# Kernel optimization log

Hardware: AMD Instinct MI355X
Metric: run time of the kernel (lower is better)

## Reference

```python
import jax, jax.numpy as jnp
import numpy as np

V, D, T_CTX, NB, H = 32000, 1024, 2048, 4, 16
HD = D // H  # head_dim (attn_dim // num_heads with attn_dim = model_dim)
B, T = 1, 2048
EPS = 1e-5


def layernorm(x, g, b):
    m = jnp.mean(x, axis=-1, keepdims=True)
    v = jnp.mean((x - m) ** 2, axis=-1, keepdims=True)
    return (x - m) * jax.lax.rsqrt(v + EPS) * g + b


def setup_inputs() -> dict:
    key = jax.random.key(0)
    ks = iter(jax.random.split(key, 64))
    s = 0.02
    inp = {
        "x": jax.random.randint(next(ks), (B, T), 0, V, dtype=jnp.int64 if jax.config.read('jax_enable_x64') else jnp.int32),
        "tok_emb": jax.random.normal(next(ks), (V, D), jnp.float32) * s,
        "pos_emb": jax.random.normal(next(ks), (T_CTX, D), jnp.float32) * s,
        # per-block stacked params, leading dim = num_blocks
        "wq": jax.random.normal(next(ks), (NB, H, D, HD), jnp.float32) * s,
        "bq": jnp.zeros((NB, H, HD), jnp.float32),
        "wk": jax.random.normal(next(ks), (NB, H, D, HD), jnp.float32) * s,
        "bk": jnp.zeros((NB, H, HD), jnp.float32),
        "wv": jax.random.normal(next(ks), (NB, H, D, HD), jnp.float32) * s,
        "bv": jnp.zeros((NB, H, HD), jnp.float32),
        "ln1_g": jnp.ones((NB, D), jnp.float32),
        "ln1_b": jnp.zeros((NB, D), jnp.float32),
        "ln2_g": jnp.ones((NB, D), jnp.float32),
        "ln2_b": jnp.zeros((NB, D), jnp.float32),
        "w1": jax.random.normal(next(ks), (NB, D, 4 * D), jnp.float32) * s,
        "b1": jnp.zeros((NB, 4 * D), jnp.float32),
        "w2": jax.random.normal(next(ks), (NB, 4 * D, D), jnp.float32) * s,
        "b2": jnp.zeros((NB, D), jnp.float32),
        "lnf_g": jnp.ones((D,), jnp.float32),
        "lnf_b": jnp.zeros((D,), jnp.float32),
        "w_vocab": jax.random.normal(next(ks), (D, V), jnp.float32) * s,
        "b_vocab": jnp.zeros((V,), jnp.float32),
    }
    return inp


def reference(x, tok_emb, pos_emb, wq, bq, wk, bk, wv, bv,
              ln1_g, ln1_b, ln2_g, ln2_b, w1, b1, w2, b2,
              lnf_g, lnf_b, w_vocab, b_vocab):
    Bb, Tt = x.shape
    h = tok_emb[x] + pos_emb[:Tt][None, :, :]  # [B,T,D]
    scale = 1.0 / jnp.sqrt(jnp.float32(D))      # NOTE: scaled by embed_dim, as in source
    causal = jnp.tril(jnp.ones((Tt, Tt), bool))
    for l in range(NB):
        xn = layernorm(h, ln1_g[l], ln1_b[l])
        q = jnp.einsum('btd,hdk->bhtk', xn, wq[l]) + bq[l][None, :, None, :]
        k = jnp.einsum('btd,hdk->bhtk', xn, wk[l]) + bk[l][None, :, None, :]
        v = jnp.einsum('btd,hdk->bhtk', xn, wv[l]) + bv[l][None, :, None, :]
        scores = jnp.einsum('bhtk,bhsk->bhts', q, k) * scale
        scores = jnp.where(causal[None, None], scores, -jnp.inf)
        probs = jax.nn.softmax(scores, axis=-1)
        attn = jnp.einsum('bhts,bhsk->bhtk', probs, v)  # [B,H,T,HD]
        attn = attn.transpose(0, 2, 1, 3).reshape(Bb, Tt, H * HD)  # head concat
        h = h + attn
        xn2 = layernorm(h, ln2_g[l], ln2_b[l])
        ff = jax.nn.relu(xn2 @ w1[l] + b1[l]) @ w2[l] + b2[l]
        h = h + ff
    h = layernorm(h, lnf_g, lnf_b)
    logits = h @ w_vocab + b_vocab  # [B,T,V]
    return logits
```

## Files before the change

### kernel.cpp

```cpp
#include <hip/hip_runtime.h>

#define TSEQ 2048
#define DM   1024
#define NBLK 4
#define NHEAD 16
#define HDIM 64
#define DFF  4096
#define NVOC 32000

typedef unsigned short u16;
typedef __attribute__((ext_vector_type(8))) short short8;
typedef __attribute__((ext_vector_type(4))) float f32x4;

__device__ float g_h[TSEQ * DM];
__device__ u16 g_xnh[TSEQ * DM];
__device__ u16 g_xnl[TSEQ * DM];
__device__ u16 g_ffh[TSEQ * DFF];
__device__ u16 g_ffl[TSEQ * DFF];
__device__ u16 g_qh[TSEQ * DM], g_ql[TSEQ * DM];
__device__ u16 g_kh[TSEQ * DM], g_kl[TSEQ * DM];
__device__ u16 g_vth[DM * TSEQ], g_vtl[DM * TSEQ];
__device__ u16 g_wqkvh[NBLK * 3 * DM * DM];
__device__ u16 g_wqkvl[NBLK * 3 * DM * DM];
__device__ u16 g_w1h[NBLK * DM * DFF];
__device__ u16 g_w1l[NBLK * DM * DFF];
__device__ u16 g_w2h[NBLK * DFF * DM];
__device__ u16 g_w2l[NBLK * DFF * DM];
__device__ u16 g_wvh[NVOC * DM];
__device__ u16 g_wvl[NVOC * DM];
__device__ float g_bqkv[NBLK * 3 * DM];

__device__ __forceinline__ u16 f2bf(float x) {
  union { float f; unsigned u; } v; v.f = x;
  unsigned r = (v.u >> 16) & 1u;
  return (u16)((v.u + 0x7fffu + r) >> 16);
}
__device__ __forceinline__ float b2f(u16 h) {
  union { float f; unsigned u; } v; v.u = ((unsigned)h) << 16; return v.f;
}
__device__ __forceinline__ void load16(const u16* g, u16* l) {
  __builtin_amdgcn_global_load_lds(
      (const __attribute__((address_space(1))) unsigned int*)(const void*)g,
      (__attribute__((address_space(3))) unsigned int*)(void*)l, 16, 0, 0);
}

__device__ __forceinline__ const u16* wsel_h(int s) {
  switch (s) { case 0: return g_wqkvh; case 1: return g_w1h;
               case 2: return g_w2h;   default: return g_wvh; }
}
__device__ __forceinline__ const u16* wsel_l(int s) {
  switch (s) { case 0: return g_wqkvl; case 1: return g_w1l;
               case 2: return g_w2l;   default: return g_wvl; }
}

__global__ __launch_bounds__(256) void embed_kernel(const int* __restrict__ x,
                                                    const float* __restrict__ tok,
                                                    const float* __restrict__ pos) {
  int t = blockIdx.x;
  const float* trow = tok + (long)x[t] * DM;
  const float* prow = pos + (long)t * DM;
  float* hrow = g_h + (long)t * DM;
  for (int i = threadIdx.x; i < DM; i += 256)
    hrow[i] = trow[i] + prow[i];
}

__global__ __launch_bounds__(256) void ln_kernel(const float* __restrict__ gamma,
                                                 const float* __restrict__ beta) {
  int t = blockIdx.x;
  const float* xr = g_h + (long)t * DM;
  float s = 0.f, ss = 0.f;
  for (int i = threadIdx.x; i < DM; i += 256) {
    float v = xr[i];
    s += v; ss += v * v;
  }
#pragma unroll
  for (int off = 32; off; off >>= 1) {
    s  += __shfl_down(s, off);
    ss += __shfl_down(ss, off);
  }
  __shared__ float red[2][4];
  int w = threadIdx.x >> 6;
  if ((threadIdx.x & 63) == 0) { red[0][w] = s; red[1][w] = ss; }
  __syncthreads();
  s  = red[0][0] + red[0][1] + red[0][2] + red[0][3];
  ss = red[1][0] + red[1][1] + red[1][2] + red[1][3];
  float mean = s * (1.f / DM);
  float var  = ss * (1.f / DM) - mean * mean;
  float rstd = rsqrtf(var + 1e-5f);
  for (int i = threadIdx.x; i < DM; i += 256) {
    float xv = (xr[i] - mean) * rstd * gamma[i] + beta[i];
    long o = (long)t * DM + i;
    u16 h = f2bf(xv);
    g_xnh[o] = h;
    g_xnl[o] = f2bf(xv - b2f(h));
  }
}

__global__ __launch_bounds__(256) void wsplit_t(const float* __restrict__ src,
                                                int dsel, long doff,
                                                int K, long sD, long sH) {
  __shared__ float tile[64][65];
  u16* dh = const_cast<u16*>(wsel_h(dsel)) + doff;
  u16* dl = const_cast<u16*>(wsel_l(dsel)) + doff;
  int n0 = blockIdx.x * 64, k0 = blockIdx.y * 64;
  int tid = threadIdx.x, ln = tid & 63, sub = tid >> 6;
  const float* sbase = src + (long)(n0 >> 6) * sH + ln;
#pragma unroll
  for (int r = 0; r < 16; ++r) {
    int kk = sub * 16 + r;
    tile[kk][ln] = sbase[(long)(k0 + kk) * sD];
  }
  __syncthreads();
#pragma unroll
  for (int r = 0; r < 16; ++r) {
    int nn = sub * 16 + r;
    float v = tile[ln][nn];
    long o = (long)(n0 + nn) * K + k0 + ln;
    u16 h = f2bf(v);
    dh[o] = h;
    dl[o] = f2bf(v - b2f(h));
  }
}

__global__ __launch_bounds__(256) void bias_qkv(const float* __restrict__ bq,
                                                const float* __restrict__ bk,
                                                const float* __restrict__ bv) {
  int i = blockIdx.x * 256 + threadIdx.x;
  int l = i / (3 * DM);
  int j = i % (3 * DM);
  const float* s = (j < DM) ? bq : (j < 2 * DM) ? bk : bv;
  g_bqkv[i] = s[(long)l * DM + (j & (DM - 1))];
}

template <int BM>
__global__ __launch_bounds__(256) void gemm_mfma(
    int aSel, int wSel, long woff,
    const float* __restrict__ biasPtr, long boff, float* __restrict__ Cout,
    int N, int K, int relu, int outmode) {
  constexpr int WR = BM / 64;
  constexpr int WC = 4 / WR;
  constexpr int NR = 128 / (16 * WC);
  __shared__ __align__(16) u16 lA[2][2][BM * 32];
  __shared__ __align__(16) u16 lB[2][2][128 * 32];

  const u16* Ah = aSel ? g_ffh : g_xnh;
  const u16* Al = aSel ? g_ffl : g_xnl;
  const u16* Bh = wsel_h(wSel) + woff;
  const u16* Bl = wsel_l(wSel) + woff;
  const float* bias = biasPtr ? biasPtr : (g_bqkv + boff);

  const int tid = threadIdx.x;
  const int w = tid >> 6, lane = tid & 63;
  const int wr = w / WC, wc = w % WC;
  const int m0 = blockIdx.x * BM;
  const int n0 = blockIdx.y * 128;
  const int klane = (lane >> 4) * 8;

  long aoff[WR], boffv[2];
#pragma unroll
  for (int i = 0; i < WR; ++i)
    aoff[i] = (long)(m0 + (i * 4 + w) * 16 + (lane & 15)) * K + klane;
#pragma unroll
  for (int i = 0; i < 2; ++i)
    boffv[i] = (long)(n0 + (i * 4 + w) * 16 + (lane & 15)) * K + klane;

  f32x4 acc[4][NR] = {};

  auto STAGE = [&](int k0, int d) {
#pragma unroll
    for (int i = 0; i < WR; ++i) {
      load16(Ah + aoff[i] + k0, &lA[d][0][(i * 4 + w) * 512]);
      load16(Al + aoff[i] + k0, &lA[d][1][(i * 4 + w) * 512]);
    }
#pragma unroll
    for (int i = 0; i < 2; ++i) {
      load16(Bh + boffv[i] + k0, &lB[d][0][(i * 4 + w) * 512]);
      load16(Bl + boffv[i] + k0, &lB[d][1][(i * 4 + w) * 512]);
    }
  };

  STAGE(0, 0);
  __syncthreads();
  int cur = 0;

  for (int k0 = 0; k0 < K; k0 += 32) {
    if (k0 + 32 < K) STAGE(k0 + 32, cur ^ 1);

    const u16* pa0 = &lA[cur][0][(wr * 4) * 512 + lane * 8];
    const u16* pa1 = &lA[cur][1][(wr * 4) * 512 + lane * 8];
    const u16* pb0 = &lB[cur][0][(wc * NR) * 512 + lane * 8];
    const u16* pb1 = &lB[cur][1][(wc * NR) * 512 + lane * 8];

    short8 a[4][2], b[NR][2];
#pragma unroll
    for (int mi = 0; mi < 4; ++mi) {
      a[mi][0] = *(const short8*)(const void*)(pa0 + mi * 512);
      a[mi][1] = *(const short8*)(const void*)(pa1 + mi * 512);
    }
#pragma unroll
    for (int ni = 0; ni < NR; ++ni) {
      b[ni][0] = *(const short8*)(const void*)(pb0 + ni * 512);
      b[ni][1] = *(const short8*)(const void*)(pb1 + ni * 512);
    }
#pragma unroll
    for (int mi = 0; mi < 4; ++mi)
#pragma unroll
      for (int ni = 0; ni < NR; ++ni) {
        acc[mi][ni] = __builtin_amdgcn_mfma_f32_16x16x32_bf16(a[mi][0], b[ni][0], acc[mi][ni], 0, 0, 0);
        acc[mi][ni] = __builtin_amdgcn_mfma_f32_16x16x32_bf16(a[mi][0], b[ni][1], acc[mi][ni], 0, 0, 0);
        acc[mi][ni] = __builtin_amdgcn_mfma_f32_16x16x32_bf16(a[mi][1], b[ni][0], acc[mi][ni], 0, 0, 0);
      }
    __syncthreads();
    cur ^= 1;
  }

#pragma unroll
  for (int mi = 0; mi < 4; ++mi)
#pragma unroll
    for (int ni = 0; ni < NR; ++ni) {
      const int col = n0 + wc * (NR * 16) + ni * 16 + (lane & 15);
      const int row0 = m0 + wr * 64 + mi * 16 + ((lane >> 4) << 2);
      const float bv = bias[col];
#pragma unroll
      for (int r = 0; r < 4; ++r) {
        float v2 = acc[mi][ni][r] + bv;
        if (relu) v2 = fmaxf(v2, 0.f);
        const long row = row0 + r;
        if (outmode == 0) {
          Cout[row * (long)N + col] = v2;
        } else if (outmode == 1) {
          long oo = row * (long)N + col;
          u16 hh = f2bf(v2);
          g_ffh[oo] = hh;
          g_ffl[oo] = f2bf(v2 - b2f(hh));
        } else if (outmode == 2) {
          u16 hh = f2bf(v2), ll = f2bf(v2 - b2f(hh));
          if (col < DM) {
            long oo = row * (long)DM + col;
            g_qh[oo] = hh; g_ql[oo] = ll;
          } else if (col < 2 * DM) {
            long oo = row * (long)DM + (col - DM);
            g_kh[oo] = hh; g_kl[oo] = ll;
          } else {
            long oo = (long)(col - 2 * DM) * TSEQ + row;
            g_vth[oo] = hh; g_vtl[oo] = ll;
          }
        } else {
          long oo = row * (long)N + col;
          g_h[oo] += v2;
        }
      }
    }
}

__global__ __launch_bounds__(256) void attn_kernel() {
  __shared__ __align__(16) u16 kbuf[2][4][2][512];
  __shared__ __align__(16) u16 vbuf[2][4][2][512];
  __shared__ __align__(16) u16 Ph[64][72];
  __shared__ __align__(16) u16 Pl[64][72];
  const int hd = blockIdx.y;
  const int q0 = blockIdx.x * 64;
  const int tid = threadIdx.x;
  const int w = tid >> 6, lane = tid & 63;
  const int grp = lane >> 4, l16 = lane & 15;
  const float scale = 0.03125f;

  short8 qf[2][2];
#pragma unroll
  for (int hl = 0; hl < 2; ++hl)
#pragma unroll
    for (int ks = 0; ks < 2; ++ks) {
      const u16* src = (hl ? g_ql : g_qh)
          + (long)(q0 + w * 16 + l16) * DM + hd * HDIM + ks * 32 + grp * 8;
      qf[hl][ks] = *(const short8*)(const void*)src;
    }

  float mrun[4] = {-1e30f, -1e30f, -1e30f, -1e30f};
  float lrun[4] = {0.f, 0.f, 0.f, 0.f};
  f32x4 o[4] = {};

  for (int s0 = 0; s0 <= q0; s0 += 64) {
    __syncthreads();
#pragma unroll
    for (int i = 0; i < 8; ++i) {
      int rid = w * 8 + i;
      int r = rid & 15;
      int hl = r >> 3, nt = (r >> 1) & 3, ks = r & 1;
      if (rid < 16) {
        const u16* src = (hl ? g_kl : g_kh)
            + (long)(s0 + nt * 16 + l16) * DM + hd * HDIM + ks * 32 + grp * 8;
        load16(src, &kbuf[hl][nt][ks][0]);
      } else {
        const u16* src = (hl ? g_vtl : g_vth)
            + (long)(hd * HDIM + nt * 16 + l16) * TSEQ + s0 + ks * 32 + grp * 8;
        load16(src, &vbuf[hl][nt][ks][0]);
      }
    }
    __syncthreads();

    f32x4 sa[4] = {};
#pragma unroll
    for (int nt = 0; nt < 4; ++nt)
#pragma unroll
      for (int ks = 0; ks < 2; ++ks) {
        short8 kh = *(const short8*)(const void*)&kbuf[0][nt][ks][lane * 8];
        short8 kl = *(const short8*)(const void*)&kbuf[1][nt][ks][lane * 8];
        sa[nt] = __builtin_amdgcn_mfma_f32_16x16x32_bf16(qf[0][ks], kh, sa[nt], 0, 0, 0);
        sa[nt] = __builtin_amdgcn_mfma_f32_16x16x32_bf16(qf[0][ks], kl, sa[nt], 0, 0, 0);
        sa[nt] = __builtin_amdgcn_mfma_f32_16x16x32_bf16(qf[1][ks], kh, sa[nt], 0, 0, 0);
      }

    float p[4][4];
#pragma unroll
    for (int nt = 0; nt < 4; ++nt)
#pragma unroll
      for (int r = 0; r < 4; ++r) {
        float sc = sa[nt][r] * scale;
        int s = s0 + nt * 16 + l16;
        int q = q0 + w * 16 + grp * 4 + r;
        p[nt][r] = (s > q) ? -1e30f : sc;
      }

#pragma unroll
    for (int r = 0; r < 4; ++r) {
      float rm = fmaxf(fmaxf(p[0][r], p[1][r]), fmaxf(p[2][r], p[3][r]));
#pragma unroll
      for (int off = 8; off; off >>= 1) rm = fmaxf(rm, __shfl_xor(rm, off));
      float mn = fmaxf(mrun[r], rm);
      float al = __expf(mrun[r] - mn);
      mrun[r] = mn;
      float ps = 0.f;
#pragma unroll
      for (int nt = 0; nt < 4; ++nt) { p[nt][r] = __expf(p[nt][r] - mn); ps += p[nt][r]; }
#pragma unroll
      for (int off = 8; off; off >>= 1) ps += __shfl_xor(ps, off);
      lrun[r] = lrun[r] * al + ps;
      o[0][r] *= al; o[1][r] *= al; o[2][r] *= al; o[3][r] *= al;
    }

#pragma unroll
    for (int nt = 0; nt < 4; ++nt)
#pragma unroll
      for (int r = 0; r < 4; ++r) {
        float pv = p[nt][r];
        u16 hh = f2bf(pv);
        Ph[w * 16 + grp * 4 + r][nt * 16 + l16] = hh;
        Pl[w * 16 + grp * 4 + r][nt * 16 + l16] = f2bf(pv - b2f(hh));
      }

#pragma unroll
    for (int ks = 0; ks < 2; ++ks) {
      short8 pah = *(const short8*)(const void*)&Ph[w * 16 + l16][ks * 32 + grp * 8];
      short8 pal = *(const short8*)(const void*)&Pl[w * 16 + l16][ks * 32 + grp * 8];
#pragma unroll
      for (int nt = 0; nt < 4; ++nt) {
        short8 vh = *(const short8*)(const void*)&vbuf[0][nt][ks][lane * 8];
        short8 vl = *(const short8*)(const void*)&vbuf[1][nt][ks][lane * 8];
        o[nt] = __builtin_amdgcn_mfma_f32_16x16x32_bf16(pah, vh, o[nt], 0, 0, 0);
        o[nt] = __builtin_amdgcn_mfma_f32_16x16x32_bf16(pah, vl, o[nt], 0, 0, 0);
        o[nt] = __builtin_amdgcn_mfma_f32_16x16x32_bf16(pal, vh, o[nt], 0, 0, 0);
      }
    }
  }

  float rl[4];
#pragma unroll
  for (int r = 0; r < 4; ++r) rl[r] = 1.f / lrun[r];
#pragma unroll
  for (int nt = 0; nt < 4; ++nt)
#pragma unroll
    for (int r = 0; r < 4; ++r)
      g_h[(long)(q0 + w * 16 + grp * 4 + r) * DM + hd * HDIM + nt * 16 + l16]
          += o[nt][r] * rl[r];
}

extern "C" void kernel_launch(void* const* d_in, const int* in_sizes, int n_in,
                              void* d_out, int out_size, void* d_ws, size_t ws_size,
                              hipStream_t stream) {
  (void)in_sizes; (void)n_in; (void)out_size; (void)d_ws; (void)ws_size;
  const int*   x    = (const int*)  d_in[0];
  const float* tok  = (const float*)d_in[1];
  const float* pos  = (const float*)d_in[2];
  const float* wq   = (const float*)d_in[3];
  const float* bq   = (const float*)d_in[4];
  const float* wk   = (const float*)d_in[5];
  const float* bk   = (const float*)d_in[6];
  const float* wv   = (const float*)d_in[7];
  const float* bv   = (const float*)d_in[8];
  const float* ln1g = (const float*)d_in[9];
  const float* ln1b = (const float*)d_in[10];
  const float* ln2g = (const float*)d_in[11];
  const float* ln2b = (const float*)d_in[12];
  const float* w1   = (const float*)d_in[13];
  const float* b1   = (const float*)d_in[14];
  const float* w2   = (const float*)d_in[15];
  const float* b2   = (const float*)d_in[16];
  const float* lnfg = (const float*)d_in[17];
  const float* lnfb = (const float*)d_in[18];
  const float* wvoc = (const float*)d_in[19];
  const float* bvoc = (const float*)d_in[20];
  float* out = (float*)d_out;

  for (int l = 0; l < NBLK; ++l) {
    long base = (long)l * 3 * DM * DM;
    wsplit_t<<<dim3(DM / 64, DM / 64), 256, 0, stream>>>(
        wq + (long)l * DM * DM, 0, base,                DM, HDIM, (long)DM * HDIM);
    wsplit_t<<<dim3(DM / 64, DM / 64), 256, 0, stream>>>(
        wk + (long)l * DM * DM, 0, base + (long)DM * DM, DM, HDIM, (long)DM * HDIM);
    wsplit_t<<<dim3(DM / 64, DM / 64), 256, 0, stream>>>(
        wv + (long)l * DM * DM, 0, base + 2L * DM * DM, DM, HDIM, (long)DM * HDIM);
    wsplit_t<<<dim3(DFF / 64, DM / 64), 256, 0, stream>>>(
        w1 + (long)l * DM * DFF, 1, (long)l * DM * DFF, DM, DFF, 64);
    wsplit_t<<<dim3(DM / 64, DFF / 64), 256, 0, stream>>>(
        w2 + (long)l * DFF * DM, 2, (long)l * DFF * DM, DFF, DM, 64);
  }
  wsplit_t<<<dim3(NVOC / 64, DM / 64), 256, 0, stream>>>(wvoc, 3, 0, DM, NVOC, 64);
  bias_qkv<<<NBLK * 3 * DM / 256, 256, 0, stream>>>(bq, bk, bv);

  embed_kernel<<<TSEQ, 256, 0, stream>>>(x, tok, pos);
  for (int l = 0; l < NBLK; ++l) {
    long base = (long)l * 3 * DM * DM;
    ln_kernel<<<TSEQ, 256, 0, stream>>>(ln1g + l * DM, ln1b + l * DM);
    gemm_mfma<64><<<dim3(TSEQ / 64, 3 * DM / 128), 256, 0, stream>>>(
        0, 0, base, nullptr, (long)l * 3 * DM, nullptr, 3 * DM, DM, 0, 2);
    attn_kernel<<<dim3(TSEQ / 64, NHEAD), 256, 0, stream>>>();
    ln_kernel<<<TSEQ, 256, 0, stream>>>(ln2g + l * DM, ln2b + l * DM);
    gemm_mfma<128><<<dim3(TSEQ / 128, DFF / 128), 256, 0, stream>>>(
        0, 1, (long)l * DM * DFF, b1 + (long)l * DFF, 0, nullptr, DFF, DM, 1, 1);
    gemm_mfma<64><<<dim3(TSEQ / 64, DM / 128), 256, 0, stream>>>(
        1, 2, (long)l * DFF * DM, b2 + (long)l * DM, 0, nullptr, DM, DFF, 0, 3);
  }
  ln_kernel<<<TSEQ, 256, 0, stream>>>(lnfg, lnfb);
  gemm_mfma<128><<<dim3(TSEQ / 128, NVOC / 128), 256, 0, stream>>>(
      0, 3, 0, bvoc, 0, out, NVOC, DM, 0, 0);
}
```

Baseline: 3.382 ms.

## Pack bf16 hi/lo split into tripled-K layout and pipeline GEMM loads

Activations and weights are stored as concatenated [hi, lo, hi] and [hi, hi, lo] along K, so the three-term bf16 split product becomes a single GEMM over 3K with one A and one B stream instead of separate hi/lo buffers. The GEMM is templated on tile sizes and wave layout, uses a double-buffer prefetch two stages ahead with explicit vmcnt waits and raw barriers, and the vocab projection gets 256x256 tiles with 512 threads. This cuts the number of separate load streams and the per-iteration sync overhead, at the cost of storing the hi part twice (more memory traffic for the packed buffers) and relying on hand-written waitcnt ordering.

```diff
diff --git a/kernel.cpp b/kernel.cpp
--- a/kernel.cpp
+++ b/kernel.cpp
@@ -13,21 +13,15 @@
 typedef __attribute__((ext_vector_type(4))) float f32x4;
 
 __device__ float g_h[TSEQ * DM];
-__device__ u16 g_xnh[TSEQ * DM];
-__device__ u16 g_xnl[TSEQ * DM];
-__device__ u16 g_ffh[TSEQ * DFF];
-__device__ u16 g_ffl[TSEQ * DFF];
+__device__ u16 g_xnp[TSEQ * 3 * DM];
+__device__ u16 g_ffp[TSEQ * 3 * DFF];
 __device__ u16 g_qh[TSEQ * DM], g_ql[TSEQ * DM];
 __device__ u16 g_kh[TSEQ * DM], g_kl[TSEQ * DM];
 __device__ u16 g_vth[DM * TSEQ], g_vtl[DM * TSEQ];
-__device__ u16 g_wqkvh[NBLK * 3 * DM * DM];
-__device__ u16 g_wqkvl[NBLK * 3 * DM * DM];
-__device__ u16 g_w1h[NBLK * DM * DFF];
-__device__ u16 g_w1l[NBLK * DM * DFF];
-__device__ u16 g_w2h[NBLK * DFF * DM];
-__device__ u16 g_w2l[NBLK * DFF * DM];
-__device__ u16 g_wvh[NVOC * DM];
-__device__ u16 g_wvl[NVOC * DM];
+__device__ u16 g_wqkvp[NBLK * 3 * DM * 3 * DM];
+__device__ u16 g_w1p[NBLK * DFF * 3 * DM];
+__device__ u16 g_w2p[NBLK * DM * 3 * DFF];
+__device__ u16 g_wvp[NVOC * 3 * DM];
 __device__ float g_bqkv[NBLK * 3 * DM];
 
 __device__ __forceinline__ u16 f2bf(float x) {
@@ -44,13 +38,16 @@
       (__attribute__((address_space(3))) unsigned int*)(void*)l, 16, 0, 0);
 }
 
-__device__ __forceinline__ const u16* wsel_h(int s) {
-  switch (s) { case 0: return g_wqkvh; case 1: return g_w1h;
-               case 2: return g_w2h;   default: return g_wvh; }
-}
-__device__ __forceinline__ const u16* wsel_l(int s) {
-  switch (s) { case 0: return g_wqkvl; case 1: return g_w1l;
-               case 2: return g_w2l;   default: return g_wvl; }
+__device__ __forceinline__ u16* wsel_p(int s) {
+  switch (s) { case 0: return g_wqkvp; case 1: return g_w1p;
+               case 2: return g_w2p;   default: return g_wvp; }
+}
+
+template <int N> __device__ __forceinline__ void waitvm() {
+  if constexpr (N == 8)      asm volatile("s_waitcnt vmcnt(8)" ::: "memory");
+  else if constexpr (N == 4) asm volatile("s_waitcnt vmcnt(4)" ::: "memory");
+  else if constexpr (N == 3) asm volatile("s_waitcnt vmcnt(3)" ::: "memory");
+  else                       asm volatile("s_waitcnt vmcnt(0)" ::: "memory");
 }
 
 __global__ __launch_bounds__(256) void embed_kernel(const int* __restrict__ x,
@@ -87,21 +84,22 @@
   float mean = s * (1.f / DM);
   float var  = ss * (1.f / DM) - mean * mean;
   float rstd = rsqrtf(var + 1e-5f);
+  u16* orow = g_xnp + (long)t * 3 * DM;
   for (int i = threadIdx.x; i < DM; i += 256) {
     float xv = (xr[i] - mean) * rstd * gamma[i] + beta[i];
-    long o = (long)t * DM + i;
     u16 h = f2bf(xv);
-    g_xnh[o] = h;
-    g_xnl[o] = f2bf(xv - b2f(h));
-  }
-}
-
-__global__ __launch_bounds__(256) void wsplit_t(const float* __restrict__ src,
-                                                int dsel, long doff,
-                                                int K, long sD, long sH) {
+    u16 lo = f2bf(xv - b2f(h));
+    orow[i] = h;
+    orow[DM + i] = lo;
+    orow[2 * DM + i] = h;
+  }
+}
+
+__global__ __launch_bounds__(256) void wpack_t(const float* __restrict__ src,
+                                               int dsel, long doff,
+                                               int K, long sD, long sH) {
   __shared__ float tile[64][65];
-  u16* dh = const_cast<u16*>(wsel_h(dsel)) + doff;
-  u16* dl = const_cast<u16*>(wsel_l(dsel)) + doff;
+  u16* dp = wsel_p(dsel) + doff;
   int n0 = blockIdx.x * 64, k0 = blockIdx.y * 64;
   int tid = threadIdx.x, ln = tid & 63, sub = tid >> 6;
   const float* sbase = src + (long)(n0 >> 6) * sH + ln;
@@ -115,10 +113,12 @@
   for (int r = 0; r < 16; ++r) {
     int nn = sub * 16 + r;
     float v = tile[ln][nn];
-    long o = (long)(n0 + nn) * K + k0 + ln;
+    long o = (long)(n0 + nn) * 3 * K + k0 + ln;
     u16 h = f2bf(v);
-    dh[o] = h;
-    dl[o] = f2bf(v - b2f(h));
+    u16 lo = f2bf(v - b2f(h));
+    dp[o] = h;
+    dp[o + K] = h;
+    dp[o + 2 * K] = lo;
   }
 }
 
@@ -132,94 +132,96 @@
   g_bqkv[i] = s[(long)l * DM + (j & (DM - 1))];
 }
 
-template <int BM>
-__global__ __launch_bounds__(256) void gemm_mfma(
+template <int BM, int BN, int BK, int WM, int WN>
+__global__ __launch_bounds__(WM * WN * 64, 2) void gemm_mfma(
     int aSel, int wSel, long woff,
     const float* __restrict__ biasPtr, long boff, float* __restrict__ Cout,
     int N, int K, int relu, int outmode) {
-  constexpr int WR = BM / 64;
-  constexpr int WC = 4 / WR;
-  constexpr int NR = 128 / (16 * WC);
-  __shared__ __align__(16) u16 lA[2][2][BM * 32];
-  __shared__ __align__(16) u16 lB[2][2][128 * 32];
-
-  const u16* Ah = aSel ? g_ffh : g_xnh;
-  const u16* Al = aSel ? g_ffl : g_xnl;
-  const u16* Bh = wsel_h(wSel) + woff;
-  const u16* Bl = wsel_l(wSel) + woff;
+  constexpr int WAVES = WM * WN;
+  constexpr int KS = BK / 32;
+  constexpr int MI = BM / (16 * WM);
+  constexpr int NI = BN / (16 * WN);
+  constexpr int CA = (BM / 16) * KS;
+  constexpr int CB = (BN / 16) * KS;
+  constexpr int L  = (CA + CB) / WAVES;
+  __shared__ __align__(16) u16 lA[2][CA * 512];
+  __shared__ __align__(16) u16 lB[2][CB * 512];
+
+  const u16* Ap = aSel ? g_ffp : g_xnp;
+  const u16* Bp = wsel_p(wSel) + woff;
   const float* bias = biasPtr ? biasPtr : (g_bqkv + boff);
 
   const int tid = threadIdx.x;
   const int w = tid >> 6, lane = tid & 63;
-  const int wr = w / WC, wc = w % WC;
+  const int wr = w / WN, wc = w % WN;
   const int m0 = blockIdx.x * BM;
-  const int n0 = blockIdx.y * 128;
-  const int klane = (lane >> 4) * 8;
-
-  long aoff[WR], boffv[2];
-#pragma unroll
-  for (int i = 0; i < WR; ++i)
-    aoff[i] = (long)(m0 + (i * 4 + w) * 16 + (lane & 15)) * K + klane;
-#pragma unroll
-  for (int i = 0; i < 2; ++i)
-    boffv[i] = (long)(n0 + (i * 4 + w) * 16 + (lane & 15)) * K + klane;
-
-  f32x4 acc[4][NR] = {};
-
-  auto STAGE = [&](int k0, int d) {
-#pragma unroll
-    for (int i = 0; i < WR; ++i) {
-      load16(Ah + aoff[i] + k0, &lA[d][0][(i * 4 + w) * 512]);
-      load16(Al + aoff[i] + k0, &lA[d][1][(i * 4 + w) * 512]);
-    }
-#pragma unroll
-    for (int i = 0; i < 2; ++i) {
-      load16(Bh + boffv[i] + k0, &lB[d][0][(i * 4 + w) * 512]);
-      load16(Bl + boffv[i] + k0, &lB[d][1][(i * 4 + w) * 512]);
+  const int n0 = blockIdx.y * BN;
+  const int grp = lane >> 4, l16 = lane & 15;
+
+  auto STAGE = [&](int kk, int d) {
+#pragma unroll
+    for (int i = 0; i < L; ++i) {
+      const int c = w * L + i;
+      if (c < CA) {
+        const int ks = c / (BM / 16), f = c % (BM / 16);
+        load16(Ap + (long)(m0 + f * 16 + (lane >> 2)) * K + kk + ks * 32 + (lane & 3) * 8,
+               &lA[d][c * 512]);
+      } else {
+        const int cb = c - CA;
+        const int ks = cb / (BN / 16), f = cb % (BN / 16);
+        load16(Bp + (long)(n0 + f * 16 + (lane >> 2)) * K + kk + ks * 32 + (lane & 3) * 8,
+               &lB[d][cb * 512]);
+      }
     }
   };
 
+  f32x4 acc[MI][NI] = {};
+
   STAGE(0, 0);
-  __syncthreads();
+  STAGE(BK, 1);
+  waitvm<L>();
+  __builtin_amdgcn_sched_barrier(0);
+  __builtin_amdgcn_s_barrier();
+
   int cur = 0;
-
-  for (int k0 = 0; k0 < K; k0 += 32) {
-    if (k0 + 32 < K) STAGE(k0 + 32, cur ^ 1);
-
-    const u16* pa0 = &lA[cur][0][(wr * 4) * 512 + lane * 8];
-    const u16* pa1 = &lA[cur][1][(wr * 4) * 512 + lane * 8];
-    const u16* pb0 = &lB[cur][0][(wc * NR) * 512 + lane * 8];
-    const u16* pb1 = &lB[cur][1][(wc * NR) * 512 + lane * 8];
-
-    short8 a[4][2], b[NR][2];
-#pragma unroll
-    for (int mi = 0; mi < 4; ++mi) {
-      a[mi][0] = *(const short8*)(const void*)(pa0 + mi * 512);
-      a[mi][1] = *(const short8*)(const void*)(pa1 + mi * 512);
-    }
-#pragma unroll
-    for (int ni = 0; ni < NR; ++ni) {
-      b[ni][0] = *(const short8*)(const void*)(pb0 + ni * 512);
-      b[ni][1] = *(const short8*)(const void*)(pb1 + ni * 512);
-    }
-#pragma unroll
-    for (int mi = 0; mi < 4; ++mi)
-#pragma unroll
-      for (int ni = 0; ni < NR; ++ni) {
-        acc[mi][ni] = __builtin_amdgcn_mfma_f32_16x16x32_bf16(a[mi][0], b[ni][0], acc[mi][ni], 0, 0, 0);
-        acc[mi][ni] = __builtin_amdgcn_mfma_f32_16x16x32_bf16(a[mi][0], b[ni][1], acc[mi][ni], 0, 0, 0);
-        acc[mi][ni] = __builtin_amdgcn_mfma_f32_16x16x32_bf16(a[mi][1], b[ni][0], acc[mi][ni], 0, 0, 0);
-      }
-    __syncthreads();
+  for (int k0 = 0; k0 < K; k0 += BK) {
+#pragma unroll
+    for (int ks = 0; ks < KS; ++ks) {
+      short8 a[MI], b[NI];
+#pragma unroll
+      for (int mi = 0; mi < MI; ++mi)
+        a[mi] = *(const short8*)(const void*)
+            &lA[cur][(ks * (BM / 16) + wr * MI + mi) * 512 + l16 * 32 + grp * 8];
+#pragma unroll
+      for (int ni = 0; ni < NI; ++ni)
+        b[ni] = *(const short8*)(const void*)
+            &lB[cur][(ks * (BN / 16) + wc * NI + ni) * 512 + l16 * 32 + grp * 8];
+#pragma unroll
+      for (int mi = 0; mi < MI; ++mi)
+#pragma unroll
+        for (int ni = 0; ni < NI; ++ni)
+          acc[mi][ni] = __builtin_amdgcn_mfma_f32_16x16x32_bf16(a[mi], b[ni], acc[mi][ni], 0, 0, 0);
+    }
+    asm volatile("s_waitcnt lgkmcnt(0)" ::: "memory");
+    __builtin_amdgcn_sched_barrier(0);
+    __builtin_amdgcn_s_barrier();
+    if (k0 + 2 * BK < K) {
+      STAGE(k0 + 2 * BK, cur);
+      waitvm<L>();
+    } else {
+      waitvm<0>();
+    }
+    __builtin_amdgcn_sched_barrier(0);
+    __builtin_amdgcn_s_barrier();
     cur ^= 1;
   }
 
 #pragma unroll
-  for (int mi = 0; mi < 4; ++mi)
-#pragma unroll
-    for (int ni = 0; ni < NR; ++ni) {
-      const int col = n0 + wc * (NR * 16) + ni * 16 + (lane & 15);
-      const int row0 = m0 + wr * 64 + mi * 16 + ((lane >> 4) << 2);
+  for (int mi = 0; mi < MI; ++mi)
+#pragma unroll
+    for (int ni = 0; ni < NI; ++ni) {
+      const int col = n0 + wc * (NI * 16) + ni * 16 + l16;
+      const int row0 = m0 + wr * (MI * 16) + mi * 16 + (grp << 2);
       const float bv = bias[col];
 #pragma unroll
       for (int r = 0; r < 4; ++r) {
@@ -229,10 +231,12 @@
         if (outmode == 0) {
           Cout[row * (long)N + col] = v2;
         } else if (outmode == 1) {
-          long oo = row * (long)N + col;
+          long oo = row * (long)(3 * N) + col;
           u16 hh = f2bf(v2);
-          g_ffh[oo] = hh;
-          g_ffl[oo] = f2bf(v2 - b2f(hh));
+          u16 ll = f2bf(v2 - b2f(hh));
+          g_ffp[oo] = hh;
+          g_ffp[oo + N] = ll;
+          g_ffp[oo + 2 * N] = hh;
         } else if (outmode == 2) {
           u16 hh = f2bf(v2), ll = f2bf(v2 - b2f(hh));
           if (col < DM) {
@@ -402,35 +406,35 @@
   float* out = (float*)d_out;
 
   for (int l = 0; l < NBLK; ++l) {
-    long base = (long)l * 3 * DM * DM;
-    wsplit_t<<<dim3(DM / 64, DM / 64), 256, 0, stream>>>(
-        wq + (long)l * DM * DM, 0, base,                DM, HDIM, (long)DM * HDIM);
-    wsplit_t<<<dim3(DM / 64, DM / 64), 256, 0, stream>>>(
-        wk + (long)l * DM * DM, 0, base + (long)DM * DM, DM, HDIM, (long)DM * HDIM);
-    wsplit_t<<<dim3(DM / 64, DM / 64), 256, 0, stream>>>(
-        wv + (long)l * DM * DM, 0, base + 2L * DM * DM, DM, HDIM, (long)DM * HDIM);
-    wsplit_t<<<dim3(DFF / 64, DM / 64), 256, 0, stream>>>(
-        w1 + (long)l * DM * DFF, 1, (long)l * DM * DFF, DM, DFF, 64);
-    wsplit_t<<<dim3(DM / 64, DFF / 64), 256, 0, stream>>>(
-        w2 + (long)l * DFF * DM, 2, (long)l * DFF * DM, DFF, DM, 64);
-  }
-  wsplit_t<<<dim3(NVOC / 64, DM / 64), 256, 0, stream>>>(wvoc, 3, 0, DM, NVOC, 64);
+    long base = (long)l * (3 * DM) * (3 * DM);
+    wpack_t<<<dim3(DM / 64, DM / 64), 256, 0, stream>>>(
+        wq + (long)l * DM * DM, 0, base,                          DM, HDIM, (long)DM * HDIM);
+    wpack_t<<<dim3(DM / 64, DM / 64), 256, 0, stream>>>(
+        wk + (long)l * DM * DM, 0, base + (long)DM * 3 * DM,      DM, HDIM, (long)DM * HDIM);
+    wpack_t<<<dim3(DM / 64, DM / 64), 256, 0, stream>>>(
+        wv + (long)l * DM * DM, 0, base + 2L * DM * 3 * DM,       DM, HDIM, (long)DM * HDIM);
+    wpack_t<<<dim3(DFF / 64, DM / 64), 256, 0, stream>>>(
+        w1 + (long)l * DM * DFF, 1, (long)l * DFF * 3 * DM, DM, DFF, 64);
+    wpack_t<<<dim3(DM / 64, DFF / 64), 256, 0, stream>>>(
+        w2 + (long)l * DFF * DM, 2, (long)l * DM * 3 * DFF, DFF, DM, 64);
+  }
+  wpack_t<<<dim3(NVOC / 64, DM / 64), 256, 0, stream>>>(wvoc, 3, 0, DM, NVOC, 64);
   bias_qkv<<<NBLK * 3 * DM / 256, 256, 0, stream>>>(bq, bk, bv);
 
   embed_kernel<<<TSEQ, 256, 0, stream>>>(x, tok, pos);
   for (int l = 0; l < NBLK; ++l) {
-    long base = (long)l * 3 * DM * DM;
+    long base = (long)l * (3 * DM) * (3 * DM);
     ln_kernel<<<TSEQ, 256, 0, stream>>>(ln1g + l * DM, ln1b + l * DM);
-    gemm_mfma<64><<<dim3(TSEQ / 64, 3 * DM / 128), 256, 0, stream>>>(
-        0, 0, base, nullptr, (long)l * 3 * DM, nullptr, 3 * DM, DM, 0, 2);
+    gemm_mfma<128, 128, 32, 2, 2><<<dim3(TSEQ / 128, 3 * DM / 128), 256, 0, stream>>>(
+        0, 0, base, nullptr, (long)l * 3 * DM, nullptr, 3 * DM, 3 * DM, 0, 2);
     attn_kernel<<<dim3(TSEQ / 64, NHEAD), 256, 0, stream>>>();
     ln_kernel<<<TSEQ, 256, 0, stream>>>(ln2g + l * DM, ln2b + l * DM);
-    gemm_mfma<128><<<dim3(TSEQ / 128, DFF / 128), 256, 0, stream>>>(
-        0, 1, (long)l * DM * DFF, b1 + (long)l * DFF, 0, nullptr, DFF, DM, 1, 1);
-    gemm_mfma<64><<<dim3(TSEQ / 64, DM / 128), 256, 0, stream>>>(
-        1, 2, (long)l * DFF * DM, b2 + (long)l * DM, 0, nullptr, DM, DFF, 0, 3);
+    gemm_mfma<128, 128, 32, 2, 2><<<dim3(TSEQ / 128, DFF / 128), 256, 0, stream>>>(
+        0, 1, (long)l * DFF * 3 * DM, b1 + (long)l * DFF, 0, nullptr, DFF, 3 * DM, 1, 1);
+    gemm_mfma<64, 128, 32, 1, 4><<<dim3(TSEQ / 64, DM / 128), 256, 0, stream>>>(
+        1, 2, (long)l * DM * 3 * DFF, b2 + (long)l * DM, 0, nullptr, DM, 3 * DFF, 0, 3);
   }
   ln_kernel<<<TSEQ, 256, 0, stream>>>(lnfg, lnfb);
-  gemm_mfma<128><<<dim3(TSEQ / 128, NVOC / 128), 256, 0, stream>>>(
-      0, 3, 0, bvoc, 0, out, NVOC, DM, 0, 0);
-}
+  gemm_mfma<256, 256, 64, 2, 4><<<dim3(TSEQ / 256, NVOC / 256), 512, 0, stream>>>(
+      0, 3, 0, bvoc, 0, out, NVOC, 3 * DM, 0, 0);
+}
```

New measurement: 3.927 ms. 1.16x slower.
